# Kernel optimization log

Measured on AMD Instinct MI355X. Metric: run time of the kernel, lower is better.

The kernel has to match this reference:

```python
import jax, jax.numpy as jnp
import numpy as np

TOP_K = 5
TRUNC = 100
EPS = 1e-07
B, T_STEPS, I_DIM, H_DIM, N_CLS = 32, 384, 64, 128, 10


def setup_inputs() -> dict:
    key = jax.random.key(0)
    ks = jax.random.split(key, 8)
    s = 1.0 / np.sqrt(H_DIM)
    u = lambda k, sh: jax.random.uniform(k, sh, jnp.float32, -s, s)
    return {
        "x": jax.random.normal(ks[0], (B, T_STEPS, I_DIM), jnp.float32),
        "W_ih": u(ks[1], (4 * H_DIM, I_DIM)),
        "W_hh": u(ks[2], (4 * H_DIM, H_DIM)),
        "b_ih": u(ks[3], (4 * H_DIM,)),
        "b_hh": u(ks[4], (4 * H_DIM,)),
        "w_t": jax.random.normal(ks[5], (2 * H_DIM, 1), jnp.float32) * 0.01,
        "W_fc": u(ks[6], (N_CLS, 2 * H_DIM)),
        "b_fc": u(ks[7], (N_CLS,)),
    }


def _lstm_cell(x_t, h, c, W_ih, W_hh, b_ih, b_hh):
    # torch.nn.LSTMCell: gate order i, f, g, o
    g = x_t @ W_ih.T + b_ih + h @ W_hh.T + b_hh
    i, f, gg, o = jnp.split(g, 4, axis=1)
    c = jax.nn.sigmoid(f) * c + jax.nn.sigmoid(i) * jnp.tanh(gg)
    h = jax.nn.sigmoid(o) * jnp.tanh(c)
    return h, c


def _sparse_attn(scores, mask, r):
    # scores: [B, T+1]; mask: valid-prefix bool [T+1]; r: traced valid length
    Bsz, L = scores.shape
    neg = jnp.where(mask[None, :], scores, -jnp.inf)

    def small(_):
        return jax.nn.softmax(neg, axis=1)

    def big(_):
        delta = jax.lax.top_k(neg, TOP_K)[0][:, -1] + EPS  # [B], k-th largest
        # faithful to torch: delta.repeat((1, r)).view(B, r) -> delta[(b*r+t) % B]
        dmat = delta[(jnp.arange(Bsz)[:, None] * r + jnp.arange(L)[None, :]) % Bsz]
        w = jnp.clip(scores - dmat, 0.0, None) * mask[None, :]
        return w / (jnp.sum(w, axis=1, keepdims=True) + EPS)

    return jax.lax.cond(r <= TOP_K, small, big, None)


def reference(x, W_ih, W_hh, b_ih, b_hh, w_t, W_fc, b_fc):
    Bsz, T, _ = x.shape
    H = W_hh.shape[1]
    dt = x.dtype
    buf0 = jnp.zeros((Bsz, T + 1, H), dt)  # h_old buffer; slot 0 (zeros) is valid
    pos = jnp.arange(T + 1)

    def step(carry, inp):
        h, c, buf = carry
        i, x_t = inp
        h, c = jax.lax.cond(
            (i + 1) % TRUNC == 0,
            lambda hc: (jax.lax.stop_gradient(hc[0]), jax.lax.stop_gradient(hc[1])),
            lambda hc: hc,
            (h, c),
        )
        h, c = _lstm_cell(x_t, h, c, W_ih, W_hh, b_ih, b_hh)
        r = i + 1  # remember_size (valid prefix of buf)
        mask = (pos < r).astype(dt)  # [T+1]
        mlp = jnp.tanh(jnp.concatenate(
            (jnp.broadcast_to(h[:, None, :], buf.shape), buf), axis=2))  # [B,T+1,2H]
        scores = (mlp @ w_t)[..., 0]  # [B, T+1]
        attn = _sparse_attn(scores, mask, r)  # [B, T+1], zero on invalid slots
        attn_c = jnp.einsum('bt,bth->bh', attn, buf)
        h = h + attn_c
        buf = jax.lax.dynamic_update_slice(buf, h[:, None, :], (0, r, 0))
        return (h, c, buf), (h, attn_c)

    init = (jnp.zeros((Bsz, H), dt), jnp.zeros((Bsz, H), dt), buf0)
    _, (hs, attn_all) = jax.lax.scan(step, init, (jnp.arange(T), jnp.swapaxes(x, 0, 1)))
    outputs = jnp.concatenate(
        (jnp.swapaxes(hs, 0, 1), jnp.swapaxes(attn_all, 0, 1)), axis=2)  # [B,T,2H]
    out = outputs @ W_fc.T + b_fc  # [B, T, num_classes]
    return out, jnp.swapaxes(hs, 0, 1)
```

## Files before the change

### kernel.cpp

```cpp
#include <hip/hip_runtime.h>
#include <stdint.h>

typedef unsigned long long u64;

#define NB   32
#define TST  384
#define IDM  64
#define HDM  128
#define NCLS 10
#define EPSF 1e-7f
#define LOG2E 1.44269504088896340736f

#define O_SBUF 0
#define O_WLDS 388
#define O_DELT 776
#define O_MISC 808
#define O_ACT  840
#define O_GEX  1032
#define O_RED  1288
#define O_IDX  2312
#define O_WFC  2696
#define O_BFC  5336
#define SMTOT  5348

__device__ __forceinline__ float sigm(float x) {
  return 1.0f / (1.0f + __builtin_amdgcn_exp2f(-LOG2E * x));
}
__device__ __forceinline__ float tanh_f(float x) {
  return 1.0f - 2.0f / (1.0f + __builtin_amdgcn_exp2f(2.0f * LOG2E * x));
}

template <int CTRL>
__device__ __forceinline__ float dppadd(float v) {
  int t = __builtin_amdgcn_update_dpp(0, __builtin_bit_cast(int, v), CTRL, 0xF, 0xF, true);
  return v + __builtin_bit_cast(float, t);
}
__device__ __forceinline__ float sum8(float v) {
  v = dppadd<0xB1>(v);
  v = dppadd<0x4E>(v);
  v = dppadd<0x141>(v);
  return v;
}
__device__ __forceinline__ float sum16(float v) {
  v = dppadd<0xB1>(v);
  v = dppadd<0x4E>(v);
  v = dppadd<0x141>(v);
  v = dppadd<0x140>(v);
  return v;
}
__device__ __forceinline__ float wave_sum(float v) {
  v = sum16(v);
  v += __shfl_xor(v, 16, 64);
  v += __shfl_xor(v, 32, 64);
  return v;
}

__device__ __forceinline__ void mail_store(u64* p, u64 v) {
  asm volatile("global_store_dwordx2 %0, %1, off sc0 sc1"
               :: "v"(p), "v"(v) : "memory");
}
__device__ __forceinline__ u64 mail_load(u64* p) {
  u64 v;
  asm volatile("global_load_dwordx2 %0, %1, off sc0 sc1\n\t"
               "s_waitcnt vmcnt(0)"
               : "=v"(v) : "v"(p) : "memory");
  return v;
}

__global__ __launch_bounds__(512, 2)
void sab_kernel(const float* __restrict__ x, const float* __restrict__ Wih,
                const float* __restrict__ Whh, const float* __restrict__ bihp,
                const float* __restrict__ bhhp, const float* __restrict__ wtp,
                const float* __restrict__ Wfcp, const float* __restrict__ bfcp,
                float* __restrict__ dout, u64* __restrict__ mail) {
  __shared__ __align__(16) float SM[SMTOT];
  int* IDX = (int*)(SM + O_IDX);

  const int tid  = threadIdx.x;
  const int lane = tid & 63;
  const int wvid = tid >> 6;
  const int b    = blockIdx.x;
  const int go   = tid >> 3;
  const int kc   = tid & 7;

  float* hsout = dout + (size_t)NB * TST * NCLS;
  const float* myx = x + (size_t)b * TST * IDM;

  float w[8][24];
  #pragma unroll
  for (int i = 0; i < 8; ++i) {
    const int g = 8 * go + i;
    #pragma unroll
    for (int j = 0; j < 24; ++j) {
      const int k = 24 * kc + j;
      w[i][j] = (k < IDM) ? Wih[g * IDM + k] : Whh[g * HDM + (k - IDM)];
    }
  }
  const float bias = bihp[tid] + bhhp[tid];

  float wt0a = 0.f, wt0b = 0.f, wt1a = 0.f, wt1b = 0.f;
  if (wvid == 0) {
    const float2 w0 = reinterpret_cast<const float2*>(wtp)[lane];
    const float2 w1 = reinterpret_cast<const float2*>(wtp + HDM)[lane];
    wt0a = w0.x; wt0b = w0.y; wt1a = w1.x; wt1b = w1.y;
  }
  float cst0 = 0.f, cst1 = 0.f, hc0 = 0.f, hc1 = 0.f;

  float t5a = 0.f, t5b = -3e38f, t5c = -3e38f, t5d = -3e38f, t5e = -3e38f;

  for (int idx = tid; idx < NCLS * 256; idx += 512)
    SM[O_WFC + (idx >> 8) * 264 + (idx & 255)] = Wfcp[idx];
  if (tid < NCLS) SM[O_BFC + tid] = bfcp[tid];
  if (tid < HDM) SM[O_ACT + 64 + tid] = 0.f;
  if (tid < IDM) SM[O_ACT + tid] = myx[tid];
  if (tid == 0) {
    SM[O_SBUF] = 0.f;
    mail_store(&mail[b], 0ull);
    mail_store(&mail[NB + b], 0ull);
  }
  __syncthreads();

  for (int t = 0; t < TST; ++t) {
    const int r = t + 1;
    const bool big = (r > 5);

    float acc[8] = {0,0,0,0,0,0,0,0};
    {
      const float4* a4 = reinterpret_cast<const float4*>(SM + O_ACT + kc * 24);
      #pragma unroll
      for (int m = 0; m < 6; ++m) {
        const float4 av = a4[m];
        #pragma unroll
        for (int i = 0; i < 8; ++i) {
          acc[i] = fmaf(av.x, w[i][4*m+0], acc[i]);
          acc[i] = fmaf(av.y, w[i][4*m+1], acc[i]);
          acc[i] = fmaf(av.z, w[i][4*m+2], acc[i]);
          acc[i] = fmaf(av.w, w[i][4*m+3], acc[i]);
        }
      }
    }
    #pragma unroll
    for (int i = 0; i < 8; ++i) acc[i] = sum8(acc[i]);
    float pre = acc[0];
    #pragma unroll
    for (int i = 1; i < 8; ++i) if (kc == i) pre = acc[i];
    pre += bias;
    const bool tg = (tid >= 256) && (tid < 384);
    SM[O_RED + tid] = tg ? tanh_f(pre) : sigm(pre);
    __syncthreads();

    if (wvid == 0) {
      __builtin_amdgcn_s_setprio(1);
      const float2 gi  = *reinterpret_cast<const float2*>(SM + O_RED + 2 * lane);
      const float2 gf  = *reinterpret_cast<const float2*>(SM + O_RED + 128 + 2 * lane);
      const float2 gg2 = *reinterpret_cast<const float2*>(SM + O_RED + 256 + 2 * lane);
      const float2 go2 = *reinterpret_cast<const float2*>(SM + O_RED + 384 + 2 * lane);
      cst0 = gf.x * cst0 + gi.x * gg2.x;
      cst1 = gf.y * cst1 + gi.y * gg2.y;
      hc0  = go2.x * tanh_f(cst0);
      hc1  = go2.y * tanh_f(cst1);
      const float sh = wave_sum(tanh_f(hc0) * wt0a + tanh_f(hc1) * wt0b);
      if (lane == 0) {
        SM[O_MISC] = sh;
        if (big) {
          const u64 pv = (((u64)(unsigned)r) << 32) | (u64)__float_as_uint(t5e + sh + EPSF);
          mail_store(&mail[(r & 1) * NB + b], pv);
        }
      }
      __builtin_amdgcn_s_setprio(0);
    } else if (wvid == 7) {
      if (big && lane < NB) {
        u64* slot = &mail[(r & 1) * NB + lane];
        u64 v = mail_load(slot);
        while ((unsigned)(v >> 32) != (unsigned)r) v = mail_load(slot);
        SM[O_DELT + lane] = __uint_as_float((unsigned)v);
      }
    } else if (wvid == 6) {
      if (t + 1 < TST && lane < IDM)
        SM[O_ACT + lane] = myx[(size_t)(t + 1) * IDM + lane];
    } else if (t > 0 && tid >= 128 && tid < 288) {
      const int cls = (tid - 128) >> 4, p = tid & 15;
      float pt = 0.f;
      #pragma unroll
      for (int i = 0; i < 16; ++i) {
        const int k = p + 16 * i;
        pt = fmaf(SM[O_WFC + cls * 264 + k], SM[O_GEX + k], pt);
      }
      pt = sum16(pt);
      if (p == 0) dout[((size_t)(b * TST + (t - 1))) * NCLS + cls] = pt + SM[O_BFC + cls];
    }
    __syncthreads();

    const float s_h = SM[O_MISC];
    float wval = 0.f;
    bool pred = false;
    if (big) {
      if (tid < r) {
        const float sc = s_h + SM[O_SBUF + tid];
        wval = fmaxf(sc - SM[O_DELT + ((b * r + tid) & (NB - 1))], 0.f);
        SM[O_WLDS + tid] = wval;
        pred = (wval > 0.f) && (tid > 0);
      }
    } else {
      float scv = (tid < r) ? (s_h + SM[O_SBUF + tid]) : -3e38f;
      float mx = scv;
      mx = fmaxf(mx, __shfl_xor(mx, 1, 64));  mx = fmaxf(mx, __shfl_xor(mx, 2, 64));
      mx = fmaxf(mx, __shfl_xor(mx, 4, 64));  mx = fmaxf(mx, __shfl_xor(mx, 8, 64));
      mx = fmaxf(mx, __shfl_xor(mx, 16, 64)); mx = fmaxf(mx, __shfl_xor(mx, 32, 64));
      if (tid < r) {
        wval = __builtin_amdgcn_exp2f(LOG2E * (scv - mx));
        SM[O_WLDS + tid] = wval;
        pred = (tid > 0);
      }
    }
    const float wsp = wave_sum(wval);
    if (lane == 0) SM[O_MISC + 8 + wvid] = wsp;
    const u64 bmask = __ballot((int)pred);
    const int cnt = (int)__popcll(bmask);
    if (pred) {
      const int pos = (int)__popcll(bmask & ((1ull << lane) - 1ull));
      IDX[(wvid << 6) + pos] = tid;
    }
    if (wvid < 6) {
      const int sub = lane >> 4;
      const int j8 = lane & 15;
      float ac0=0.f,ac1=0.f,ac2=0.f,ac3=0.f,ac4=0.f,ac5=0.f,ac6=0.f,ac7=0.f;
      for (int rk = sub; rk < cnt; rk += 4) {
        const int tp = IDX[(wvid << 6) + rk];
        const float wgt = SM[O_WLDS + tp];
        const float* bp = hsout + ((size_t)(b * TST + tp - 1)) * HDM + j8 * 8;
        const float4 v0 = *reinterpret_cast<const float4*>(bp);
        const float4 v1 = *reinterpret_cast<const float4*>(bp + 4);
        ac0 = fmaf(wgt, v0.x, ac0); ac1 = fmaf(wgt, v0.y, ac1);
        ac2 = fmaf(wgt, v0.z, ac2); ac3 = fmaf(wgt, v0.w, ac3);
        ac4 = fmaf(wgt, v1.x, ac4); ac5 = fmaf(wgt, v1.y, ac5);
        ac6 = fmaf(wgt, v1.z, ac6); ac7 = fmaf(wgt, v1.w, ac7);
      }
      ac0 += __shfl_xor(ac0,16,64); ac0 += __shfl_xor(ac0,32,64);
      ac1 += __shfl_xor(ac1,16,64); ac1 += __shfl_xor(ac1,32,64);
      ac2 += __shfl_xor(ac2,16,64); ac2 += __shfl_xor(ac2,32,64);
      ac3 += __shfl_xor(ac3,16,64); ac3 += __shfl_xor(ac3,32,64);
      ac4 += __shfl_xor(ac4,16,64); ac4 += __shfl_xor(ac4,32,64);
      ac5 += __shfl_xor(ac5,16,64); ac5 += __shfl_xor(ac5,32,64);
      ac6 += __shfl_xor(ac6,16,64); ac6 += __shfl_xor(ac6,32,64);
      ac7 += __shfl_xor(ac7,16,64); ac7 += __shfl_xor(ac7,32,64);
      if (sub == 0) {
        float4* r4 = reinterpret_cast<float4*>(SM + O_RED + wvid * 128 + j8 * 8);
        r4[0] = make_float4(ac0, ac1, ac2, ac3);
        r4[1] = make_float4(ac4, ac5, ac6, ac7);
      }
    }
    __syncthreads();

    if (wvid == 0) {
      float wsum = 0.f;
      #pragma unroll
      for (int i = 0; i < 8; ++i) wsum += SM[O_MISC + 8 + i];
      const float inv = 1.0f / (wsum + (big ? EPSF : 0.0f));
      float s0 = 0.f, s1 = 0.f;
      #pragma unroll
      for (int wv2 = 0; wv2 < 6; ++wv2) {
        const float2 p2 = reinterpret_cast<const float2*>(SM + O_RED + wv2 * 128)[lane];
        s0 += p2.x; s1 += p2.y;
      }
      const float at0 = s0 * inv, at1 = s1 * inv;
      const float hf0 = hc0 + at0, hf1 = hc1 + at1;
      const float2 hv = make_float2(hf0, hf1);
      reinterpret_cast<float2*>(hsout + (size_t)(b * TST + t) * HDM)[lane] = hv;
      reinterpret_cast<float2*>(SM + O_ACT + 64)[lane] = hv;
      reinterpret_cast<float2*>(SM + O_GEX)[lane] = hv;
      reinterpret_cast<float2*>(SM + O_GEX + 128)[lane] = make_float2(at0, at1);
      if (r < TST) {
        const float tb = wave_sum(tanh_f(hf0) * wt1a + tanh_f(hf1) * wt1b);
        if (lane == 0) SM[O_SBUF + r] = tb;
        if (tb > t5e) {
          if (tb > t5a)      { t5e=t5d; t5d=t5c; t5c=t5b; t5b=t5a; t5a=tb; }
          else if (tb > t5b) { t5e=t5d; t5d=t5c; t5c=t5b; t5b=tb; }
          else if (tb > t5c) { t5e=t5d; t5d=t5c; t5c=tb; }
          else if (tb > t5d) { t5e=t5d; t5d=tb; }
          else               { t5e=tb; }
        }
      }
    }
    __syncthreads();
  }

  if (tid < 160) {
    const int cls = tid >> 4, p = tid & 15;
    float pt = 0.f;
    #pragma unroll
    for (int i = 0; i < 16; ++i) {
      const int k = p + 16 * i;
      pt = fmaf(SM[O_WFC + cls * 264 + k], SM[O_GEX + k], pt);
    }
    pt = sum16(pt);
    if (p == 0) dout[((size_t)(b * TST + (TST - 1))) * NCLS + cls] = pt + SM[O_BFC + cls];
  }
}

extern "C" void kernel_launch(void* const* d_in, const int* in_sizes, int n_in,
                              void* d_out, int out_size, void* d_ws, size_t ws_size,
                              hipStream_t stream) {
  const float* x   = (const float*)d_in[0];
  const float* Wih = (const float*)d_in[1];
  const float* Whh = (const float*)d_in[2];
  const float* bih = (const float*)d_in[3];
  const float* bhh = (const float*)d_in[4];
  const float* wt  = (const float*)d_in[5];
  const float* Wfc = (const float*)d_in[6];
  const float* bfc = (const float*)d_in[7];
  sab_kernel<<<dim3(NB), dim3(512), 0, stream>>>(
      x, Wih, Whh, bih, bhh, wt, Wfc, bfc, (float*)d_out, (u64*)d_ws);
}
```

Measured before the change: 1.929 ms.

## Drop per-step barrier by computing h in every wave and prefetching x-projection

Every wave now computes the final h for the step redundantly and keeps it in registers, feeding the W_hh product through cross-lane shuffles instead of an LDS activation buffer. This removes the trailing __syncthreads per timestep. The x·W_ih partial for the next step is computed early, before the barrier, so only the 128-wide recurrent part sits on the critical path. Gate outputs and the cell h move to dedicated LDS regions so nothing races without that barrier. Launch bounds drop to one block per CU and setprio is removed. The cost is redundant per-wave work and extra shuffle traffic.

```diff
diff --git a/kernel.cpp b/kernel.cpp
--- a/kernel.cpp
+++ b/kernel.cpp
@@ -15,13 +15,15 @@
 #define O_WLDS 388
 #define O_DELT 776
 #define O_MISC 808
-#define O_ACT  840
-#define O_GEX  1032
-#define O_RED  1288
-#define O_IDX  2312
-#define O_WFC  2696
-#define O_BFC  5336
-#define SMTOT  5348
+#define O_HC   824
+#define O_ACT  952
+#define O_GEX  1016
+#define O_GEXC 1272
+#define O_RED  1784
+#define O_IDX  2552
+#define O_WFC  2936
+#define O_BFC  5576
+#define SMTOT  5588
 
 __device__ __forceinline__ float sigm(float x) {
   return 1.0f / (1.0f + __builtin_amdgcn_exp2f(-LOG2E * x));
@@ -67,7 +69,7 @@
   return v;
 }
 
-__global__ __launch_bounds__(512, 2)
+__global__ __launch_bounds__(512, 1)
 void sab_kernel(const float* __restrict__ x, const float* __restrict__ Wih,
                 const float* __restrict__ Whh, const float* __restrict__ bihp,
                 const float* __restrict__ bhhp, const float* __restrict__ wtp,
@@ -91,10 +93,9 @@
   for (int i = 0; i < 8; ++i) {
     const int g = 8 * go + i;
     #pragma unroll
-    for (int j = 0; j < 24; ++j) {
-      const int k = 24 * kc + j;
-      w[i][j] = (k < IDM) ? Wih[g * IDM + k] : Whh[g * HDM + (k - IDM)];
-    }
+    for (int j = 0; j < 8; ++j)  w[i][j]     = Wih[g * IDM + 8 * kc + j];
+    #pragma unroll
+    for (int j = 0; j < 16; ++j) w[i][8 + j] = Whh[g * HDM + 16 * kc + j];
   }
   const float bias = bihp[tid] + bhhp[tid];
 
@@ -104,14 +105,14 @@
     const float2 w1 = reinterpret_cast<const float2*>(wtp + HDM)[lane];
     wt0a = w0.x; wt0b = w0.y; wt1a = w1.x; wt1b = w1.y;
   }
-  float cst0 = 0.f, cst1 = 0.f, hc0 = 0.f, hc1 = 0.f;
+  float cst0 = 0.f, cst1 = 0.f;
+  float hv0 = 0.f, hv1 = 0.f;
 
   float t5a = 0.f, t5b = -3e38f, t5c = -3e38f, t5d = -3e38f, t5e = -3e38f;
 
   for (int idx = tid; idx < NCLS * 256; idx += 512)
     SM[O_WFC + (idx >> 8) * 264 + (idx & 255)] = Wfcp[idx];
   if (tid < NCLS) SM[O_BFC + tid] = bfcp[tid];
-  if (tid < HDM) SM[O_ACT + 64 + tid] = 0.f;
   if (tid < IDM) SM[O_ACT + tid] = myx[tid];
   if (tid == 0) {
     SM[O_SBUF] = 0.f;
@@ -120,23 +121,37 @@
   }
   __syncthreads();
 
+  float accx[8];
+  {
+    const float4* a4 = reinterpret_cast<const float4*>(SM + O_ACT + 8 * kc);
+    const float4 av0 = a4[0], av1 = a4[1];
+    #pragma unroll
+    for (int i = 0; i < 8; ++i) {
+      float a = 0.f;
+      a = fmaf(av0.x, w[i][0], a); a = fmaf(av0.y, w[i][1], a);
+      a = fmaf(av0.z, w[i][2], a); a = fmaf(av0.w, w[i][3], a);
+      a = fmaf(av1.x, w[i][4], a); a = fmaf(av1.y, w[i][5], a);
+      a = fmaf(av1.z, w[i][6], a); a = fmaf(av1.w, w[i][7], a);
+      accx[i] = a;
+    }
+  }
+
   for (int t = 0; t < TST; ++t) {
     const int r = t + 1;
     const bool big = (r > 5);
 
-    float acc[8] = {0,0,0,0,0,0,0,0};
-    {
-      const float4* a4 = reinterpret_cast<const float4*>(SM + O_ACT + kc * 24);
-      #pragma unroll
-      for (int m = 0; m < 6; ++m) {
-        const float4 av = a4[m];
-        #pragma unroll
-        for (int i = 0; i < 8; ++i) {
-          acc[i] = fmaf(av.x, w[i][4*m+0], acc[i]);
-          acc[i] = fmaf(av.y, w[i][4*m+1], acc[i]);
-          acc[i] = fmaf(av.z, w[i][4*m+2], acc[i]);
-          acc[i] = fmaf(av.w, w[i][4*m+3], acc[i]);
-        }
+    float acc[8];
+    #pragma unroll
+    for (int i = 0; i < 8; ++i) acc[i] = accx[i];
+    #pragma unroll
+    for (int c = 0; c < 8; ++c) {
+      const int src = 8 * kc + c;
+      const float h0 = __shfl(hv0, src, 64);
+      const float h1 = __shfl(hv1, src, 64);
+      #pragma unroll
+      for (int i = 0; i < 8; ++i) {
+        acc[i] = fmaf(h0, w[i][8 + 2 * c], acc[i]);
+        acc[i] = fmaf(h1, w[i][9 + 2 * c], acc[i]);
       }
     }
     #pragma unroll
@@ -146,19 +161,19 @@
     for (int i = 1; i < 8; ++i) if (kc == i) pre = acc[i];
     pre += bias;
     const bool tg = (tid >= 256) && (tid < 384);
-    SM[O_RED + tid] = tg ? tanh_f(pre) : sigm(pre);
+    SM[O_GEXC + tid] = tg ? tanh_f(pre) : sigm(pre);
     __syncthreads();
 
     if (wvid == 0) {
-      __builtin_amdgcn_s_setprio(1);
-      const float2 gi  = *reinterpret_cast<const float2*>(SM + O_RED + 2 * lane);
-      const float2 gf  = *reinterpret_cast<const float2*>(SM + O_RED + 128 + 2 * lane);
-      const float2 gg2 = *reinterpret_cast<const float2*>(SM + O_RED + 256 + 2 * lane);
-      const float2 go2 = *reinterpret_cast<const float2*>(SM + O_RED + 384 + 2 * lane);
+      const float2 gi  = *reinterpret_cast<const float2*>(SM + O_GEXC + 2 * lane);
+      const float2 gf  = *reinterpret_cast<const float2*>(SM + O_GEXC + 128 + 2 * lane);
+      const float2 gg2 = *reinterpret_cast<const float2*>(SM + O_GEXC + 256 + 2 * lane);
+      const float2 go2 = *reinterpret_cast<const float2*>(SM + O_GEXC + 384 + 2 * lane);
       cst0 = gf.x * cst0 + gi.x * gg2.x;
       cst1 = gf.y * cst1 + gi.y * gg2.y;
-      hc0  = go2.x * tanh_f(cst0);
-      hc1  = go2.y * tanh_f(cst1);
+      const float hc0 = go2.x * tanh_f(cst0);
+      const float hc1 = go2.y * tanh_f(cst1);
+      *reinterpret_cast<float2*>(SM + O_HC + 2 * lane) = make_float2(hc0, hc1);
       const float sh = wave_sum(tanh_f(hc0) * wt0a + tanh_f(hc1) * wt0b);
       if (lane == 0) {
         SM[O_MISC] = sh;
@@ -167,7 +182,6 @@
           mail_store(&mail[(r & 1) * NB + b], pv);
         }
       }
-      __builtin_amdgcn_s_setprio(0);
     } else if (wvid == 7) {
       if (big && lane < NB) {
         u64* slot = &mail[(r & 1) * NB + lane];
@@ -198,7 +212,6 @@
       if (tid < r) {
         const float sc = s_h + SM[O_SBUF + tid];
         wval = fmaxf(sc - SM[O_DELT + ((b * r + tid) & (NB - 1))], 0.f);
-        SM[O_WLDS + tid] = wval;
         pred = (wval > 0.f) && (tid > 0);
       }
     } else {
@@ -209,10 +222,10 @@
       mx = fmaxf(mx, __shfl_xor(mx, 16, 64)); mx = fmaxf(mx, __shfl_xor(mx, 32, 64));
       if (tid < r) {
         wval = __builtin_amdgcn_exp2f(LOG2E * (scv - mx));
-        SM[O_WLDS + tid] = wval;
         pred = (tid > 0);
       }
     }
+    if (tid < r) SM[O_WLDS + tid] = wval;
     const float wsp = wave_sum(wval);
     if (lane == 0) SM[O_MISC + 8 + wvid] = wsp;
     const u64 bmask = __ballot((int)pred);
@@ -250,13 +263,27 @@
         r4[1] = make_float4(ac4, ac5, ac6, ac7);
       }
     }
+    {
+      const float4* a4 = reinterpret_cast<const float4*>(SM + O_ACT + 8 * kc);
+      const float4 av0 = a4[0], av1 = a4[1];
+      #pragma unroll
+      for (int i = 0; i < 8; ++i) {
+        float a = 0.f;
+        a = fmaf(av0.x, w[i][0], a); a = fmaf(av0.y, w[i][1], a);
+        a = fmaf(av0.z, w[i][2], a); a = fmaf(av0.w, w[i][3], a);
+        a = fmaf(av1.x, w[i][4], a); a = fmaf(av1.y, w[i][5], a);
+        a = fmaf(av1.z, w[i][6], a); a = fmaf(av1.w, w[i][7], a);
+        accx[i] = a;
+      }
+    }
     __syncthreads();
 
-    if (wvid == 0) {
+    {
       float wsum = 0.f;
       #pragma unroll
       for (int i = 0; i < 8; ++i) wsum += SM[O_MISC + 8 + i];
       const float inv = 1.0f / (wsum + (big ? EPSF : 0.0f));
+      const float2 hcv = *reinterpret_cast<const float2*>(SM + O_HC + 2 * lane);
       float s0 = 0.f, s1 = 0.f;
       #pragma unroll
       for (int wv2 = 0; wv2 < 6; ++wv2) {
@@ -264,27 +291,29 @@
         s0 += p2.x; s1 += p2.y;
       }
       const float at0 = s0 * inv, at1 = s1 * inv;
-      const float hf0 = hc0 + at0, hf1 = hc1 + at1;
-      const float2 hv = make_float2(hf0, hf1);
-      reinterpret_cast<float2*>(hsout + (size_t)(b * TST + t) * HDM)[lane] = hv;
-      reinterpret_cast<float2*>(SM + O_ACT + 64)[lane] = hv;
-      reinterpret_cast<float2*>(SM + O_GEX)[lane] = hv;
-      reinterpret_cast<float2*>(SM + O_GEX + 128)[lane] = make_float2(at0, at1);
-      if (r < TST) {
-        const float tb = wave_sum(tanh_f(hf0) * wt1a + tanh_f(hf1) * wt1b);
-        if (lane == 0) SM[O_SBUF + r] = tb;
-        if (tb > t5e) {
-          if (tb > t5a)      { t5e=t5d; t5d=t5c; t5c=t5b; t5b=t5a; t5a=tb; }
-          else if (tb > t5b) { t5e=t5d; t5d=t5c; t5c=t5b; t5b=tb; }
-          else if (tb > t5c) { t5e=t5d; t5d=t5c; t5c=tb; }
-          else if (tb > t5d) { t5e=t5d; t5d=tb; }
-          else               { t5e=tb; }
+      hv0 = hcv.x + at0;
+      hv1 = hcv.y + at1;
+      if (wvid == 0) {
+        reinterpret_cast<float2*>(hsout + (size_t)(b * TST + t) * HDM)[lane] =
+            make_float2(hv0, hv1);
+        reinterpret_cast<float2*>(SM + O_GEX)[lane] = make_float2(hv0, hv1);
+        reinterpret_cast<float2*>(SM + O_GEX + 128)[lane] = make_float2(at0, at1);
+        if (r < TST) {
+          const float tb = wave_sum(tanh_f(hv0) * wt1a + tanh_f(hv1) * wt1b);
+          if (lane == 0) SM[O_SBUF + r] = tb;
+          if (tb > t5e) {
+            if (tb > t5a)      { t5e=t5d; t5d=t5c; t5c=t5b; t5b=t5a; t5a=tb; }
+            else if (tb > t5b) { t5e=t5d; t5d=t5c; t5c=t5b; t5b=tb; }
+            else if (tb > t5c) { t5e=t5d; t5d=t5c; t5c=tb; }
+            else if (tb > t5d) { t5e=t5d; t5d=tb; }
+            else               { t5e=tb; }
+          }
         }
       }
     }
-    __syncthreads();
-  }
-
+  }
+
+  __syncthreads();
   if (tid < 160) {
     const int cls = tid >> 4, p = tid & 15;
     float pt = 0.f;
```

Result: no change. 1.950 ms (+1.1%).
